# Kernel tuning notes

Measured on AMD Instinct MI355X. Metric: run time of the kernel, lower is better.

## Reference

```python
import jax, jax.numpy as jnp
import numpy as np

N, D, M = 65536, 64, 4096

def setup_inputs() -> dict:
    key = jax.random.key(0)
    k1, k2 = jax.random.split(key)
    p = jax.random.normal(k1, (N, D), dtype=jnp.float32)
    c = jax.random.normal(k2, (M, D), dtype=jnp.float32)
    pn = jnp.sum(p * p, axis=1, keepdims=True)        # [N, 1]
    c_sq = jnp.sum(c * c, axis=1, keepdims=True).T     # [1, M]
    return {"p": p, "pn": pn, "c": c, "c_sq": c_sq}

def reference(p, pn, c, c_sq):
    # dist[n, m] = ||p_n||^2 + ||c_m||^2 - 2 <p_n, c_m>
    pc = jnp.matmul(p, c.T) * 2.0                      # [N, M]
    dist = pn + c_sq - pc                              # broadcast add -> [N, M]
    min_dists = jnp.min(dist, axis=1)                  # [N]
    min_labels = jnp.argmin(dist, axis=1)              # [N] int
    return (min_dists, min_labels)
```

## Files before the change

kernel.cpp:

```cpp
#include <hip/hip_runtime.h>
#include <math.h>

constexpr int N_ = 65536;
constexpr int D_ = 64;
constexpr int M_ = 4096;
constexpr int Q_ = 4;
constexpr int TQ = M_ / Q_ / 16;
constexpr int GT = 2;
constexpr int NG = TQ / GT;

typedef __attribute__((ext_vector_type(8))) short  short8;
typedef __attribute__((ext_vector_type(4))) float  f32x4;

__device__ inline unsigned long long pack_dl(float d, unsigned m) {
    return ((unsigned long long)__float_as_uint(d) << 32) | m;
}
__device__ inline unsigned short f2bf(float x) {
    union { float f; unsigned u; } v; v.f = x;
    return (unsigned short)((v.u + 0x7fffu + ((v.u >> 16) & 1u)) >> 16);
}
__device__ inline unsigned umin32(unsigned a, unsigned b) { return a < b ? a : b; }
__device__ inline unsigned umax32(unsigned a, unsigned b) { return a > b ? a : b; }

__device__ inline short8 load_bf8(const float* src) {
    float4 x = *reinterpret_cast<const float4*>(src);
    float4 y = *reinterpret_cast<const float4*>(src + 4);
    unsigned short o[8] = {f2bf(x.x), f2bf(x.y), f2bf(x.z), f2bf(x.w),
                           f2bf(y.x), f2bf(y.y), f2bf(y.z), f2bf(y.w)};
    return *reinterpret_cast<short8*>(o);
}

__global__ __launch_bounds__(256) void pwd_prep(
        const float* __restrict__ c, const float* __restrict__ c_sq,
        unsigned short* __restrict__ ChiT, float* __restrict__ nhcsq) {
    const int tid = blockIdx.x * 256 + threadIdx.x;
    constexpr int CT = M_ * D_ / 8;
    if (tid < CT) {
        const int id  = tid;
        const int col = id & 15;
        const int g4  = (id >> 4) & 3;
        const int ks  = (id >> 6) & 1;
        const int t   = id >> 7;
        short8 v = load_bf8(c + (size_t)(t * 16 + col) * D_ + ks * 32 + g4 * 8);
        *reinterpret_cast<short8*>(ChiT + (size_t)id * 8) = v;
    } else if (tid < CT + M_) {
        const int m = tid - CT;
        nhcsq[m] = -0.5f * c_sq[m];
    }
}

__global__ __launch_bounds__(256, 8) void pwd_scan(
        const float* __restrict__ p,
        const float* __restrict__ pn,
        const unsigned short* __restrict__ ChiT,
        const float* __restrict__ nhcsq,
        unsigned* __restrict__ candk) {
    __shared__ __align__(16) char  lds_chi[2][GT * 2048];
    __shared__ __align__(16) float nh_lds[1024];

    const int tid  = threadIdx.x;
    const int lane = tid & 63;
    const int wav  = tid >> 6;
    const int col  = lane & 15;
    const int g4   = lane >> 4;
    const int quarter = blockIdx.y;
    const int pbase   = blockIdx.x * 128 + wav * 32;

    reinterpret_cast<float4*>(nh_lds)[tid] =
        reinterpret_cast<const float4*>(nhcsq + quarter * 1024)[tid];

    short8 bfr[2][2];
#pragma unroll
    for (int g = 0; g < 2; ++g)
#pragma unroll
        for (int ks = 0; ks < 2; ++ks)
            bfr[g][ks] = load_bf8(
                p + (size_t)(pbase + g * 16 + col) * D_ + ks * 32 + g4 * 8);

    float pn2[2];
#pragma unroll
    for (int g = 0; g < 2; ++g)
        pn2[g] = 0.5f * pn[pbase + g * 16 + col] + 1.0f;

    unsigned k0[2][2], k1[2][2];
#pragma unroll
    for (int g = 0; g < 2; ++g)
#pragma unroll
        for (int tr = 0; tr < 2; ++tr) { k0[g][tr] = 0xFFFFFFFFu; k1[g][tr] = 0xFFFFFFFFu; }

    const char* gchi = reinterpret_cast<const char*>(ChiT) + (size_t)quarter * TQ * 2048;

#define STAGE_LOAD(R, grp) \
    R = *reinterpret_cast<const float4*>(gchi + (size_t)(grp) * (GT * 2048) + tid * 16);

#define STAGE_WRITE(BUF, R) \
    *reinterpret_cast<float4*>(lds_chi[BUF] + tid * 16) = R;

#define COMPUTE_GROUP(BUF, grp)                                                  \
    _Pragma("unroll")                                                            \
    for (int t = 0; t < GT; ++t) {                                               \
        const char* tb = lds_chi[BUF] + t * 2048;                                \
        const short8 a0 = *reinterpret_cast<const short8*>(tb + g4*256 + col*16);\
        const short8 a1 = *reinterpret_cast<const short8*>(tb + 1024 + g4*256 + col*16); \
        const int tg = (grp) * GT + t;                                           \
        const float4 q = *reinterpret_cast<const float4*>(nh_lds + tg*16 + g4*4);\
        const unsigned mb = (unsigned)(quarter * 1024 + tg * 16 + g4 * 4);       \
        _Pragma("unroll")                                                        \
        for (int g = 0; g < 2; ++g) {                                            \
            f32x4 acc = {q.x, q.y, q.z, q.w};                                    \
            acc = __builtin_amdgcn_mfma_f32_16x16x32_bf16(a0, bfr[g][0], acc, 0, 0, 0); \
            acc = __builtin_amdgcn_mfma_f32_16x16x32_bf16(a1, bfr[g][1], acc, 0, 0, 0); \
            _Pragma("unroll")                                                    \
            for (int r = 0; r < 4; ++r) {                                        \
                const int tr = r >> 1;                                           \
                const float keyf = pn2[g] - acc[r];              \
                const unsigned key = (__float_as_uint(keyf) & 0xFFFFF000u)       \
                                     | (mb + r);                   \
                const unsigned t0 = k0[g][tr];                                   \
                k0[g][tr] = umin32(t0, key);                                     \
                k1[g][tr] = umin32(k1[g][tr], umax32(t0, key));                  \
            }                                                                    \
        }                                                                        \
    }

    float4 rA, rB;
    STAGE_LOAD(rA, 0)
    __syncthreads();

#pragma unroll 1
    for (int gp = 0; gp < NG; gp += 2) {
        STAGE_WRITE(0, rA)
        __syncthreads();
        STAGE_LOAD(rB, gp + 1)
        COMPUTE_GROUP(0, gp)

        STAGE_WRITE(1, rB)
        __syncthreads();
        if (gp + 2 < NG) { STAGE_LOAD(rA, gp + 2) }
        COMPUTE_GROUP(1, gp + 1)
    }

#pragma unroll
    for (int g = 0; g < 2; ++g) {
        const int pt = pbase + g * 16 + col;
        uint4 w;
        w.x = k0[g][0]; w.y = k1[g][0]; w.z = k0[g][1]; w.w = k1[g][1];
        *reinterpret_cast<uint4*>(
            candk + ((size_t)(quarter * N_ + pt) * 16 + g4 * 4)) = w;
    }
#undef STAGE_LOAD
#undef STAGE_WRITE
#undef COMPUTE_GROUP
}

__global__ __launch_bounds__(256) void pwd_exact(
        const float* __restrict__ p, const float* __restrict__ pn,
        const float* __restrict__ c, const float* __restrict__ c_sq,
        const unsigned* __restrict__ candk, float* __restrict__ out) {
    const int t  = blockIdx.x * 256 + threadIdx.x;
    const int pt = t >> 2, q = t & 3;

    const uint4* kw = reinterpret_cast<const uint4*>(candk + ((size_t)q * N_ + pt) * 16);
    uint4 w0 = kw[0], w1 = kw[1], w2 = kw[2], w3 = kw[3];
    const unsigned ks[16] = {w0.x, w0.y, w0.z, w0.w, w1.x, w1.y, w1.z, w1.w,
                             w2.x, w2.y, w2.z, w2.w, w3.x, w3.y, w3.z, w3.w};
    unsigned mn = ks[0];
#pragma unroll
    for (int i = 1; i < 16; ++i) mn = umin32(mn, ks[i]);
    mn = umin32(mn, (unsigned)__shfl_xor((int)mn, 1));
    mn = umin32(mn, (unsigned)__shfl_xor((int)mn, 2));
    const float thr = __uint_as_float(mn & 0xFFFFF000u) + 1.5f;

    bool any = false;
#pragma unroll
    for (int i = 0; i < 16; ++i)
        any |= (__uint_as_float(ks[i] & 0xFFFFF000u) <= thr);

    unsigned long long best = ~0ull;
    if (any) {
        float pr[D_];
        const float4* p4 = reinterpret_cast<const float4*>(p + (size_t)pt * D_);
#pragma unroll
        for (int i = 0; i < D_ / 4; ++i) {
            float4 v = p4[i];
            pr[4*i+0] = v.x; pr[4*i+1] = v.y; pr[4*i+2] = v.z; pr[4*i+3] = v.w;
        }
        const float pnn = pn[pt];
#pragma unroll 1
        for (int i = 0; i < 16; ++i) {
            if (__uint_as_float(ks[i] & 0xFFFFF000u) > thr) continue;
            const unsigned m = ks[i] & 0xFFFu;
            const float* cm = c + (size_t)m * D_;
            float a0 = 0.f, a1 = 0.f, a2 = 0.f, a3 = 0.f;
#pragma unroll
            for (int k = 0; k < D_; k += 4) {
                a0 = fmaf(pr[k+0], cm[k+0], a0);
                a1 = fmaf(pr[k+1], cm[k+1], a1);
                a2 = fmaf(pr[k+2], cm[k+2], a2);
                a3 = fmaf(pr[k+3], cm[k+3], a3);
            }
            const float dot  = (a0 + a1) + (a2 + a3);
            const float dist = fmaf(-2.f, dot, pnn + c_sq[m]);
            const unsigned long long key = pack_dl(dist, m);
            best = key < best ? key : best;
        }
    }
    unsigned long long o1 = __shfl_xor(best, 1); best = o1 < best ? o1 : best;
    unsigned long long o2 = __shfl_xor(best, 2); best = o2 < best ? o2 : best;
    if (q == 0) {
        out[pt]      = __uint_as_float((unsigned)(best >> 32));
        out[N_ + pt] = (float)(unsigned)(best & 0xffffffffu);
    }
}

constexpr int FCH = 8;
constexpr int FMC = M_ / FCH;

__global__ __launch_bounds__(256) void pwd_chunk(
        const float* __restrict__ p, const float* __restrict__ pn,
        const float* __restrict__ c, const float* __restrict__ c_sq,
        unsigned long long* __restrict__ ws) {
    const int n = blockIdx.x * 256 + threadIdx.x;
    const int mbase = blockIdx.y * FMC;
    float prr[D_];
    const float4* p4 = reinterpret_cast<const float4*>(p + (size_t)n * D_);
#pragma unroll
    for (int i = 0; i < D_ / 4; ++i) {
        float4 v = p4[i];
        prr[4*i+0] = v.x; prr[4*i+1] = v.y; prr[4*i+2] = v.z; prr[4*i+3] = v.w;
    }
    const float pnn = pn[n];
    float bestD = INFINITY;
    int   bestM = mbase;
#pragma unroll 2
    for (int mi = 0; mi < FMC; ++mi) {
        const int m = mbase + mi;
        const float* cm = c + (size_t)m * D_;
        float a0 = 0.f, a1 = 0.f, a2 = 0.f, a3 = 0.f;
#pragma unroll
        for (int k = 0; k < D_; k += 4) {
            a0 = fmaf(prr[k+0], cm[k+0], a0);
            a1 = fmaf(prr[k+1], cm[k+1], a1);
            a2 = fmaf(prr[k+2], cm[k+2], a2);
            a3 = fmaf(prr[k+3], cm[k+3], a3);
        }
        const float dot  = (a0 + a1) + (a2 + a3);
        const float dist = fmaf(-2.f, dot, pnn + c_sq[m]);
        if (dist < bestD) { bestD = dist; bestM = m; }
    }
    atomicMin(&ws[n], pack_dl(bestD, (unsigned)bestM));
}

__global__ __launch_bounds__(256) void pwd_out(
        const unsigned long long* __restrict__ results, float* __restrict__ out) {
    const int n = blockIdx.x * 256 + threadIdx.x;
    const unsigned long long v = results[n];
    out[n]      = __uint_as_float((unsigned)(v >> 32));
    out[N_ + n] = (float)(unsigned)(v & 0xffffffffu);
}

extern "C" void kernel_launch(void* const* d_in, const int* in_sizes, int n_in,
                              void* d_out, int out_size, void* d_ws, size_t ws_size,
                              hipStream_t stream) {
    const float* p    = (const float*)d_in[0];
    const float* pn   = (const float*)d_in[1];
    const float* c    = (const float*)d_in[2];
    const float* c_sq = (const float*)d_in[3];
    float* out = (float*)d_out;

    char* ws = (char*)d_ws;
    const size_t off_chi  = 0;
    const size_t off_nhc  = (size_t)M_ * D_ * 2;
    const size_t off_cand = off_nhc + (size_t)M_ * 4;
    const size_t need     = off_cand + (size_t)Q_ * N_ * 16 * 4;

    if (ws_size >= need) {
        unsigned short* ChiT  = (unsigned short*)(ws + off_chi);
        float*          nhcsq = (float*)(ws + off_nhc);
        unsigned*       candk = (unsigned*)(ws + off_cand);

        constexpr int PREP_T = M_ * D_ / 8 + M_;
        pwd_prep<<<(PREP_T + 255) / 256, 256, 0, stream>>>(c, c_sq, ChiT, nhcsq);
        dim3 sgrid(N_ / 128, Q_);
        pwd_scan<<<sgrid, 256, 0, stream>>>(p, pn, ChiT, nhcsq, candk);
        pwd_exact<<<(N_ * 4) / 256, 256, 0, stream>>>(p, pn, c, c_sq, candk, out);
    } else if (ws_size >= (size_t)N_ * 8) {
        unsigned long long* results = (unsigned long long*)ws;
        hipMemsetAsync(ws, 0xFF, (size_t)N_ * 8, stream);
        dim3 grid(N_ / 256, FCH);
        pwd_chunk<<<grid, 256, 0, stream>>>(p, pn, c, c_sq, results);
        pwd_out<<<N_ / 256, 256, 0, stream>>>(results, out);
    }
}
```

Baseline: 159.9 us.

## Read centroid tiles directly from global memory instead of LDS double-buffering

The scan kernel drops its LDS staging of centroid bf16 tiles and the -0.5*c_sq values, along with the block barriers. Each wave now loads MFMA A-operands and bias directly from global memory, relying on L1/L2 caching because all waves read the same tiles. Separately, the exact-refinement kernel builds a bitmask of surviving candidates and walks it with ffs, re-reading the candidate index from global memory instead of scanning all 16 with a branch. This removes barrier stalls and LDS traffic, but global load latency is now exposed unless the unroll-by-2 hides it.

```diff
diff --git a/kernel.cpp b/kernel.cpp
--- a/kernel.cpp
+++ b/kernel.cpp
@@ -6,8 +6,6 @@
 constexpr int M_ = 4096;
 constexpr int Q_ = 4;
 constexpr int TQ = M_ / Q_ / 16;
-constexpr int GT = 2;
-constexpr int NG = TQ / GT;
 
 typedef __attribute__((ext_vector_type(8))) short  short8;
 typedef __attribute__((ext_vector_type(4))) float  f32x4;
@@ -55,19 +53,12 @@
         const unsigned short* __restrict__ ChiT,
         const float* __restrict__ nhcsq,
         unsigned* __restrict__ candk) {
-    __shared__ __align__(16) char  lds_chi[2][GT * 2048];
-    __shared__ __align__(16) float nh_lds[1024];
-
     const int tid  = threadIdx.x;
     const int lane = tid & 63;
-    const int wav  = tid >> 6;
     const int col  = lane & 15;
     const int g4   = lane >> 4;
     const int quarter = blockIdx.y;
-    const int pbase   = blockIdx.x * 128 + wav * 32;
-
-    reinterpret_cast<float4*>(nh_lds)[tid] =
-        reinterpret_cast<const float4*>(nhcsq + quarter * 1024)[tid];
+    const int pbase   = blockIdx.x * 128 + (tid >> 6) * 32;
 
     short8 bfr[2][2];
 #pragma unroll
@@ -88,56 +79,32 @@
 #pragma unroll
         for (int tr = 0; tr < 2; ++tr) { k0[g][tr] = 0xFFFFFFFFu; k1[g][tr] = 0xFFFFFFFFu; }
 
-    const char* gchi = reinterpret_cast<const char*>(ChiT) + (size_t)quarter * TQ * 2048;
-
-#define STAGE_LOAD(R, grp) \
-    R = *reinterpret_cast<const float4*>(gchi + (size_t)(grp) * (GT * 2048) + tid * 16);
-
-#define STAGE_WRITE(BUF, R) \
-    *reinterpret_cast<float4*>(lds_chi[BUF] + tid * 16) = R;
-
-#define COMPUTE_GROUP(BUF, grp)                                                  \
-    _Pragma("unroll")                                                            \
-    for (int t = 0; t < GT; ++t) {                                               \
-        const char* tb = lds_chi[BUF] + t * 2048;                                \
-        const short8 a0 = *reinterpret_cast<const short8*>(tb + g4*256 + col*16);\
-        const short8 a1 = *reinterpret_cast<const short8*>(tb + 1024 + g4*256 + col*16); \
-        const int tg = (grp) * GT + t;                                           \
-        const float4 q = *reinterpret_cast<const float4*>(nh_lds + tg*16 + g4*4);\
-        const unsigned mb = (unsigned)(quarter * 1024 + tg * 16 + g4 * 4);       \
-        _Pragma("unroll")                                                        \
-        for (int g = 0; g < 2; ++g) {                                            \
-            f32x4 acc = {q.x, q.y, q.z, q.w};                                    \
-            acc = __builtin_amdgcn_mfma_f32_16x16x32_bf16(a0, bfr[g][0], acc, 0, 0, 0); \
-            acc = __builtin_amdgcn_mfma_f32_16x16x32_bf16(a1, bfr[g][1], acc, 0, 0, 0); \
-            _Pragma("unroll")                                                    \
-            for (int r = 0; r < 4; ++r) {                                        \
-                const int tr = r >> 1;                                           \
-                const float keyf = pn2[g] - acc[r];              \
-                const unsigned key = (__float_as_uint(keyf) & 0xFFFFF000u)       \
-                                     | (mb + r);                   \
-                const unsigned t0 = k0[g][tr];                                   \
-                k0[g][tr] = umin32(t0, key);                                     \
-                k1[g][tr] = umin32(k1[g][tr], umax32(t0, key));                  \
-            }                                                                    \
-        }                                                                        \
-    }
-
-    float4 rA, rB;
-    STAGE_LOAD(rA, 0)
-    __syncthreads();
-
-#pragma unroll 1
-    for (int gp = 0; gp < NG; gp += 2) {
-        STAGE_WRITE(0, rA)
-        __syncthreads();
-        STAGE_LOAD(rB, gp + 1)
-        COMPUTE_GROUP(0, gp)
-
-        STAGE_WRITE(1, rB)
-        __syncthreads();
-        if (gp + 2 < NG) { STAGE_LOAD(rA, gp + 2) }
-        COMPUTE_GROUP(1, gp + 1)
+    const char*  gchi = reinterpret_cast<const char*>(ChiT) + (size_t)quarter * TQ * 2048;
+    const float* nhq  = nhcsq + quarter * 1024;
+
+#pragma unroll 2
+    for (int t = 0; t < TQ; ++t) {
+        const char* tb = gchi + (size_t)t * 2048;
+        const short8 a0 = *reinterpret_cast<const short8*>(tb + g4 * 256 + col * 16);
+        const short8 a1 = *reinterpret_cast<const short8*>(tb + 1024 + g4 * 256 + col * 16);
+        const float4 q  = *reinterpret_cast<const float4*>(nhq + t * 16 + g4 * 4);
+        const unsigned mb = (unsigned)(quarter * 1024 + t * 16 + g4 * 4);
+#pragma unroll
+        for (int g = 0; g < 2; ++g) {
+            f32x4 acc = {q.x, q.y, q.z, q.w};
+            acc = __builtin_amdgcn_mfma_f32_16x16x32_bf16(a0, bfr[g][0], acc, 0, 0, 0);
+            acc = __builtin_amdgcn_mfma_f32_16x16x32_bf16(a1, bfr[g][1], acc, 0, 0, 0);
+#pragma unroll
+            for (int r = 0; r < 4; ++r) {
+                const int tr = r >> 1;
+                const float keyf = pn2[g] - acc[r];
+                const unsigned key = (__float_as_uint(keyf) & 0xFFFFF000u)
+                                     | (mb + r);
+                const unsigned t0 = k0[g][tr];
+                k0[g][tr] = umin32(t0, key);
+                k1[g][tr] = umin32(k1[g][tr], umax32(t0, key));
+            }
+        }
     }
 
 #pragma unroll
@@ -148,9 +115,6 @@
         *reinterpret_cast<uint4*>(
             candk + ((size_t)(quarter * N_ + pt) * 16 + g4 * 4)) = w;
     }
-#undef STAGE_LOAD
-#undef STAGE_WRITE
-#undef COMPUTE_GROUP
 }
 
 __global__ __launch_bounds__(256) void pwd_exact(
@@ -171,13 +135,13 @@
     mn = umin32(mn, (unsigned)__shfl_xor((int)mn, 2));
     const float thr = __uint_as_float(mn & 0xFFFFF000u) + 1.5f;
 
-    bool any = false;
+    unsigned mask = 0;
 #pragma unroll
     for (int i = 0; i < 16; ++i)
-        any |= (__uint_as_float(ks[i] & 0xFFFFF000u) <= thr);
+        mask |= (__uint_as_float(ks[i] & 0xFFFFF000u) <= thr) ? (1u << i) : 0u;
 
     unsigned long long best = ~0ull;
-    if (any) {
+    if (mask) {
         float pr[D_];
         const float4* p4 = reinterpret_cast<const float4*>(p + (size_t)pt * D_);
 #pragma unroll
@@ -186,10 +150,10 @@
             pr[4*i+0] = v.x; pr[4*i+1] = v.y; pr[4*i+2] = v.z; pr[4*i+3] = v.w;
         }
         const float pnn = pn[pt];
-#pragma unroll 1
-        for (int i = 0; i < 16; ++i) {
-            if (__uint_as_float(ks[i] & 0xFFFFF000u) > thr) continue;
-            const unsigned m = ks[i] & 0xFFFu;
+        while (mask) {
+            const int i = __ffs(mask) - 1;
+            mask &= mask - 1;
+            const unsigned m = candk[((size_t)q * N_ + pt) * 16 + i] & 0xFFFu;
             const float* cm = c + (size_t)m * D_;
             float a0 = 0.f, a1 = 0.f, a2 = 0.f, a3 = 0.f;
 #pragma unroll
```

After: 154.0 us. 3.7% less time.
